# Performance work log

Hardware: AMD Instinct MI355X
Metric: run time of the kernel (lower is better)

The kernel has to match this reference:

```python
import jax, jax.numpy as jnp
import numpy as np

B, T, C = 2, 2048, 1024
NUM_HEADS = 16
HEAD_DIM = C // NUM_HEADS
TEMP = 1.0
LN_EPS = 1e-6


def setup_inputs() -> dict:
    key = jax.random.key(0)
    kx, kqw, kpw = jax.random.split(key, 3)
    x = jax.random.normal(kx, (B, T, C), dtype=jnp.float32)
    # causal mask, broadcastable to [B, H, T, T]
    mask = jnp.tril(jnp.ones((T, T), dtype=bool))[None, None, :, :]
    # LayerNorm params (flax defaults: scale=1, bias=0)
    ln_scale = jnp.ones((C,), dtype=jnp.float32)
    ln_bias = jnp.zeros((C,), dtype=jnp.float32)
    # xavier_uniform init for dense kernels, zero bias (torch_linear)
    lim_qkv = float(np.sqrt(6.0 / (C + 3 * C)))
    qkv_w = jax.random.uniform(kqw, (C, 3 * C), jnp.float32, -lim_qkv, lim_qkv)
    qkv_b = jnp.zeros((3 * C,), dtype=jnp.float32)
    lim_p = float(np.sqrt(6.0 / (C + C)))
    proj_w = jax.random.uniform(kpw, (C, C), jnp.float32, -lim_p, lim_p)
    proj_b = jnp.zeros((C,), dtype=jnp.float32)
    return {"x": x, "mask": mask, "ln_scale": ln_scale, "ln_bias": ln_bias,
            "qkv_w": qkv_w, "qkv_b": qkv_b, "proj_w": proj_w, "proj_b": proj_b}


def reference(x, mask, ln_scale, ln_bias, qkv_w, qkv_b, proj_w, proj_b):
    b, t, c = x.shape
    # LayerNorm (eps=1e-6, flax default)
    mu = jnp.mean(x, axis=-1, keepdims=True)
    var = jnp.mean(jnp.square(x - mu), axis=-1, keepdims=True)
    xn = (x - mu) * jax.lax.rsqrt(var + LN_EPS) * ln_scale + ln_bias
    # fused QKV projection
    qkv = xn @ qkv_w + qkv_b
    q, k, v = jnp.split(qkv, 3, axis=-1)
    q = q.reshape(b, t, NUM_HEADS, HEAD_DIM) / TEMP
    k = k.reshape(b, t, NUM_HEADS, HEAD_DIM)
    v = v.reshape(b, t, NUM_HEADS, HEAD_DIM)
    # scaled dot-product attention with mask (eval path: no dropout)
    q = q / jnp.sqrt(jnp.float32(HEAD_DIM)).astype(x.dtype)
    scores = jnp.einsum('bqhd,bkhd->bhqk', q, k)  # [B,H,T,T]
    big_neg = jnp.finfo(x.dtype).min
    scores = jnp.where(mask, scores, big_neg)
    attn_weights = jax.nn.softmax(scores, axis=-1).astype(x.dtype)
    out = jnp.einsum('bhqk,bkhd->bqhd', attn_weights, v).reshape(b, t, c)
    return out @ proj_w + proj_b
```

## Files before the change

kernel.cpp:

```cpp
#include <hip/hip_runtime.h>
#include <cstdint>

#define DEV __device__ __forceinline__

typedef unsigned int u32;
typedef unsigned short u16;
typedef __attribute__((ext_vector_type(4))) float f32x4;
typedef __attribute__((ext_vector_type(4))) u32 u32x4;
typedef __attribute__((ext_vector_type(2))) u32 u32x2;
typedef __attribute__((ext_vector_type(8))) __bf16 bf16x8;

static_assert(sizeof(bf16x8) == 16, "bf16x8 must be 16B");

static constexpr int Tn = 2048, Cn = 1024;
static constexpr int Mrows = 2 * Tn;

DEV u16 f2bf_rne(float f) {
  u32 u = __builtin_bit_cast(u32, f);
  u32 r = u + 0x7fffu + ((u >> 16) & 1u);
  return (u16)(r >> 16);
}
DEV float bf2f(u16 h) {
  u32 u = ((u32)h) << 16;
  return __builtin_bit_cast(float, u);
}
DEV u32 pack2bf(float a, float b) {
  return (u32)f2bf_rne(a) | ((u32)f2bf_rne(b) << 16);
}

DEV void stage16(const void* g, void* l) {
#if __has_builtin(__builtin_amdgcn_global_load_lds)
  __builtin_amdgcn_global_load_lds(
      (__attribute__((address_space(1))) u32*)(uintptr_t)g,
      (__attribute__((address_space(3))) u32*)l, 16, 0, 0);
#else
  *(u32x4*)l = *(const u32x4*)g;
#endif
}

__global__ __launch_bounds__(256) void ln_kernel(const float* __restrict__ x,
                                                 const float* __restrict__ sc,
                                                 const float* __restrict__ bi,
                                                 u16* __restrict__ xn) {
  int row = blockIdx.x;
  int t = threadIdx.x;
  const float* xr = x + (size_t)row * Cn;
  f32x4 v = *(const f32x4*)(xr + t * 4);
  float s = v.x + v.y + v.z + v.w;
  float s2 = v.x * v.x + v.y * v.y + v.z * v.z + v.w * v.w;
#pragma unroll
  for (int off = 1; off < 64; off <<= 1) {
    s += __shfl_xor(s, off);
    s2 += __shfl_xor(s2, off);
  }
  __shared__ float red[8];
  if ((t & 63) == 0) {
    red[(t >> 6) * 2] = s;
    red[(t >> 6) * 2 + 1] = s2;
  }
  __syncthreads();
  s = red[0] + red[2] + red[4] + red[6];
  s2 = red[1] + red[3] + red[5] + red[7];
  float mean = s * (1.0f / Cn);
  float var = s2 * (1.0f / Cn) - mean * mean;
  float rstd = rsqrtf(var + 1e-6f);
  f32x4 g = *(const f32x4*)(sc + t * 4);
  f32x4 b = *(const f32x4*)(bi + t * 4);
  u32 lo = pack2bf((v.x - mean) * rstd * g.x + b.x, (v.y - mean) * rstd * g.y + b.y);
  u32 hi = pack2bf((v.z - mean) * rstd * g.z + b.z, (v.w - mean) * rstd * g.w + b.w);
  u32x2 pack = {lo, hi};
  *(u32x2*)(xn + (size_t)row * Cn + t * 4) = pack;
}

__global__ __launch_bounds__(256) void transpose_cast(const float* __restrict__ src,
                                                      u16* __restrict__ dst,
                                                      int R, int Cc) {
  __shared__ float tile[32][33];
  int tx = threadIdx.x, ty = threadIdx.y;
  int c0 = blockIdx.x * 32, r0 = blockIdx.y * 32;
#pragma unroll
  for (int k = 0; k < 4; ++k)
    tile[ty + 8 * k][tx] = src[(size_t)(r0 + ty + 8 * k) * Cc + c0 + tx];
  __syncthreads();
#pragma unroll
  for (int k = 0; k < 4; ++k)
    dst[(size_t)(c0 + ty + 8 * k) * R + r0 + tx] = f2bf_rne(tile[tx][ty + 8 * k]);
}

__global__ __launch_bounds__(256) void vt_prep(const u16* __restrict__ qkvm,
                                               u16* __restrict__ vt) {
  __shared__ u16 tile[32][33];
  int bh = blockIdx.z;
  int b = bh >> 4, h = bh & 15;
  int t0 = blockIdx.x * 32, d0 = blockIdx.y * 32;
  int tx = threadIdx.x, ty = threadIdx.y;
#pragma unroll
  for (int k = 0; k < 4; ++k)
    tile[ty + 8 * k][tx] =
        qkvm[(size_t)(b * Tn + t0 + ty + 8 * k) * 3072 + 2 * Cn + h * 64 + d0 + tx];
  __syncthreads();
#pragma unroll
  for (int k = 0; k < 4; ++k)
    vt[((size_t)bh * 64 + d0 + ty + 8 * k) * 2048 + t0 + tx] = tile[tx][ty + 8 * k];
}

template <bool OUT_F32, bool QKV_SCALE>
__global__ __launch_bounds__(256, 2) void gemm_kernel(const u16* __restrict__ A,
                                                      const u16* __restrict__ Bt,
                                                      const float* __restrict__ bias,
                                                      void* __restrict__ Cout,
                                                      int Nsz, int Ksz) {
  __shared__ u16 As[128 * 32];
  __shared__ u16 Bs[128 * 32];
  int t = threadIdx.x;
  int l = t & 63, w = t >> 6;
  int quad = l >> 4, c16 = l & 15;
  int wm = w & 1, wn = w >> 1;
  int m0 = blockIdx.y * 128, n0 = blockIdx.x * 128;

  f32x4 acc[4][4];
#pragma unroll
  for (int mt = 0; mt < 4; ++mt)
#pragma unroll
    for (int nt = 0; nt < 4; ++nt) acc[mt][nt] = (f32x4){0.f, 0.f, 0.f, 0.f};

  for (int kk = 0; kk < Ksz; kk += 32) {
#pragma unroll
    for (int i = 0; i < 2; ++i) {
      int c = t + i * 256;
      int m = c >> 2, k8 = (c & 3) ^ ((m >> 1) & 3);
      stage16(A + (size_t)(m0 + m) * Ksz + kk + k8 * 8, (char*)As + c * 16);
    }
#pragma unroll
    for (int i = 0; i < 2; ++i) {
      int c = t + i * 256;
      int n = c >> 2, k8 = (c & 3) ^ ((n >> 1) & 3);
      stage16(Bt + (size_t)(n0 + n) * Ksz + kk + k8 * 8, (char*)Bs + c * 16);
    }
    __syncthreads();
    bf16x8 af[4], bf[4];
#pragma unroll
    for (int mt = 0; mt < 4; ++mt) {
      int m = wm * 64 + mt * 16 + c16;
      int LC = m * 4 + (quad ^ ((m >> 1) & 3));
      af[mt] = *(const bf16x8*)((const char*)As + LC * 16);
    }
#pragma unroll
    for (int nt = 0; nt < 4; ++nt) {
      int n = wn * 64 + nt * 16 + c16;
      int LC = n * 4 + (quad ^ ((n >> 1) & 3));
      bf[nt] = *(const bf16x8*)((const char*)Bs + LC * 16);
    }
#pragma unroll
    for (int mt = 0; mt < 4; ++mt)
#pragma unroll
      for (int nt = 0; nt < 4; ++nt)
        acc[mt][nt] = __builtin_amdgcn_mfma_f32_16x16x32_bf16(af[mt], bf[nt],
                                                              acc[mt][nt], 0, 0, 0);
    __syncthreads();
  }
#pragma unroll
  for (int mt = 0; mt < 4; ++mt) {
    int row = m0 + wm * 64 + mt * 16 + quad * 4;
#pragma unroll
    for (int nt = 0; nt < 4; ++nt) {
      int col = n0 + wn * 64 + nt * 16 + c16;
      float bv = bias[col];
      float scale = (QKV_SCALE && col < 1024) ? 0.125f : 1.0f;
#pragma unroll
      for (int r = 0; r < 4; ++r) {
        float v = (acc[mt][nt][r] + bv) * scale;
        if (OUT_F32)
          ((float*)Cout)[(size_t)(row + r) * Nsz + col] = v;
        else
          ((u16*)Cout)[(size_t)(row + r) * Nsz + col] = f2bf_rne(v);
      }
    }
  }
}

__constant__ int4 chunk_tab[24] = {
    {15, 0, 8, 0}, {15, 8, 8, 1}, {14, 0, 8, 0}, {7, 0, 8, -1},
    {14, 8, 7, 1}, {13, 0, 7, 0}, {13, 7, 7, 1}, {12, 0, 7, 0}, {6, 0, 7, -1},
    {12, 7, 6, 1}, {11, 0, 6, 0}, {11, 6, 6, 1}, {10, 0, 6, 0}, {5, 0, 6, -1},
    {10, 6, 5, 1}, {9, 0, 5, 0}, {9, 5, 5, 1}, {8, 0, 5, 0}, {4, 0, 5, -1},
    {8, 5, 4, 1}, {3, 0, 4, -1},
    {2, 0, 3, -1},
    {1, 0, 2, -1},
    {0, 0, 1, -1}};

__global__ __launch_bounds__(256, 2) void flash_kernel(const u16* __restrict__ qkv,
                                                       const u16* __restrict__ vt,
                                                       u16* __restrict__ aout,
                                                       u16* __restrict__ Op,
                                                       float* __restrict__ ml) {
  int4 ck = chunk_tab[blockIdx.x >> 5];
  int bh = blockIdx.x & 31;
  int qt = ck.x, k0 = ck.y, kend = ck.y + ck.z, half = ck.w;
  int b = bh >> 4, h = bh & 15;
  int t = threadIdx.x, l = t & 63, w = t >> 6;
  int quad = l >> 4, c16 = l & 15;
  int q0 = qt * 128;

  __shared__ u16 Ks[128 * 64];
  __shared__ u16 Vs[64 * 128];
  __shared__ u16 Ps[128 * 128];

  bf16x8 qf[2][2];
#pragma unroll
  for (int nt = 0; nt < 2; ++nt)
#pragma unroll
    for (int ks = 0; ks < 2; ++ks)
      qf[nt][ks] = *(const bf16x8*)(qkv +
          (size_t)(b * Tn + q0 + w * 32 + nt * 16 + c16) * 3072 +
          h * 64 + ks * 32 + quad * 8);

  float mrow[2] = {-1e30f, -1e30f};
  float lrow[2] = {0.f, 0.f};
  f32x4 o[2][4];
#pragma unroll
  for (int mq = 0; mq < 2; ++mq)
#pragma unroll
    for (int dt = 0; dt < 4; ++dt) o[mq][dt] = (f32x4){0.f, 0.f, 0.f, 0.f};

  for (int kt = k0; kt < kend; ++kt) {
#pragma unroll
    for (int i = 0; i < 4; ++i) {
      int c = t + i * 256;
      int key = c >> 3, d8 = (c & 7) ^ (key & 7);
      stage16(qkv + (size_t)(b * Tn + kt * 128 + key) * 3072 + Cn + h * 64 + d8 * 8,
              (char*)Ks + c * 16);
    }
#pragma unroll
    for (int i = 0; i < 4; ++i) {
      int c = t + i * 256;
      int d = c >> 4, k8 = (c & 15) ^ (d & 15);
      stage16(vt + ((size_t)bh * 64 + d) * 2048 + kt * 128 + k8 * 8,
              (char*)Vs + c * 16);
    }
    __syncthreads();

    f32x4 s[8][2];
#pragma unroll
    for (int mt = 0; mt < 8; ++mt)
#pragma unroll
      for (int nt = 0; nt < 2; ++nt) s[mt][nt] = (f32x4){0.f, 0.f, 0.f, 0.f};
#pragma unroll
    for (int mt = 0; mt < 8; ++mt) {
#pragma unroll
      for (int ks = 0; ks < 2; ++ks) {
        int key = mt * 16 + c16;
        int d8 = ks * 4 + quad;
        int LC = key * 8 + (d8 ^ (key & 7));
        bf16x8 kf = *(const bf16x8*)((const char*)Ks + LC * 16);
#pragma unroll
        for (int nt = 0; nt < 2; ++nt)
          s[mt][nt] = __builtin_amdgcn_mfma_f32_16x16x32_bf16(kf, qf[nt][ks],
                                                              s[mt][nt], 0, 0, 0);
      }
    }
    if (kt == qt) {
#pragma unroll
      for (int mt = 0; mt < 8; ++mt)
#pragma unroll
        for (int nt = 0; nt < 2; ++nt)
#pragma unroll
          for (int r = 0; r < 4; ++r) {
            int key = kt * 128 + mt * 16 + quad * 4 + r;
            int q = q0 + w * 32 + nt * 16 + c16;
            if (key > q) s[mt][nt][r] = -1e30f;
          }
    }
    float alph[2];
#pragma unroll
    for (int nt = 0; nt < 2; ++nt) {
      float rm = -1e30f;
#pragma unroll
      for (int mt = 0; mt < 8; ++mt)
#pragma unroll
        for (int r = 0; r < 4; ++r) rm = fmaxf(rm, s[mt][nt][r]);
      rm = fmaxf(rm, __shfl_xor(rm, 16));
      rm = fmaxf(rm, __shfl_xor(rm, 32));
      float mnew = fmaxf(mrow[nt], rm);
      alph[nt] = __expf(mrow[nt] - mnew);
      mrow[nt] = mnew;
      float rs = 0.f;
#pragma unroll
      for (int mt = 0; mt < 8; ++mt)
#pragma unroll
        for (int r = 0; r < 4; ++r) {
          float e = __expf(s[mt][nt][r] - mnew);
          s[mt][nt][r] = e;
          rs += e;
        }
      rs += __shfl_xor(rs, 16);
      rs += __shfl_xor(rs, 32);
      lrow[nt] = lrow[nt] * alph[nt] + rs;
    }
#pragma unroll
    for (int mq = 0; mq < 2; ++mq)
#pragma unroll
      for (int r = 0; r < 4; ++r) {
        float a = __shfl(alph[mq], quad * 4 + r);
#pragma unroll
        for (int dt = 0; dt < 4; ++dt) o[mq][dt][r] *= a;
      }
#pragma unroll
    for (int mt = 0; mt < 8; ++mt)
#pragma unroll
      for (int nt = 0; nt < 2; ++nt) {
        int q = w * 32 + nt * 16 + c16;
        int kc = mt * 4 + quad;
        int LC = q * 32 + (kc ^ ((q & 15) << 1));
        u32x2 pk = {pack2bf(s[mt][nt][0], s[mt][nt][1]),
                    pack2bf(s[mt][nt][2], s[mt][nt][3])};
        *(u32x2*)((char*)Ps + LC * 8) = pk;
      }
#pragma unroll
    for (int ks = 0; ks < 4; ++ks) {
      bf16x8 pa[2];
#pragma unroll
      for (int mq = 0; mq < 2; ++mq) {
        int q = w * 32 + mq * 16 + c16;
        int kc = ks * 8 + quad * 2;
        int LC = q * 32 + (kc ^ ((q & 15) << 1));
        pa[mq] = *(const bf16x8*)((const char*)Ps + LC * 8);
      }
#pragma unroll
      for (int dt = 0; dt < 4; ++dt) {
        int d = dt * 16 + c16;
        int vc = d * 16 + ((ks * 4 + quad) ^ (d & 15));
        bf16x8 vf = *(const bf16x8*)((const char*)Vs + vc * 16);
#pragma unroll
        for (int mq = 0; mq < 2; ++mq)
          o[mq][dt] = __builtin_amdgcn_mfma_f32_16x16x32_bf16(pa[mq], vf, o[mq][dt],
                                                              0, 0, 0);
      }
    }
    __syncthreads();
  }

  float linv[2] = {1.0f / lrow[0], 1.0f / lrow[1]};
  if (half < 0) {
#pragma unroll
    for (int mq = 0; mq < 2; ++mq)
#pragma unroll
      for (int r = 0; r < 4; ++r) {
        float li = __shfl(linv[mq], quad * 4 + r);
        int q = q0 + w * 32 + mq * 16 + quad * 4 + r;
#pragma unroll
        for (int dt = 0; dt < 4; ++dt)
          aout[(size_t)(b * Tn + q) * 1024 + h * 64 + dt * 16 + c16] =
              f2bf_rne(o[mq][dt][r] * li);
      }
  } else {
    int ps = ((qt - 8) * 32 + bh) * 2 + half;
#pragma unroll
    for (int mq = 0; mq < 2; ++mq)
#pragma unroll
      for (int r = 0; r < 4; ++r) {
        float li = __shfl(linv[mq], quad * 4 + r);
        int qr = w * 32 + mq * 16 + quad * 4 + r;
#pragma unroll
        for (int dt = 0; dt < 4; ++dt)
          Op[((size_t)ps * 128 + qr) * 64 + dt * 16 + c16] =
              f2bf_rne(o[mq][dt][r] * li);
      }
    if (quad == 0) {
#pragma unroll
      for (int nt = 0; nt < 2; ++nt) {
        int qr = w * 32 + nt * 16 + c16;
        ml[((size_t)ps * 128 + qr) * 2] = mrow[nt];
        ml[((size_t)ps * 128 + qr) * 2 + 1] = lrow[nt];
      }
    }
  }
}

__global__ __launch_bounds__(256) void combine_kernel(const u16* __restrict__ Op,
                                                      const float* __restrict__ ml,
                                                      u16* __restrict__ aout) {
  int qt = 8 + (blockIdx.x >> 5);
  int bh = blockIdx.x & 31;
  int b = bh >> 4, h = bh & 15;
  int ps0 = ((qt - 8) * 32 + bh) * 2;
  int d = threadIdx.x & 63, rq = threadIdx.x >> 6;
  for (int r = 0; r < 32; ++r) {
    int row = rq * 32 + r;
    float m0 = ml[((size_t)ps0 * 128 + row) * 2];
    float l0 = ml[((size_t)ps0 * 128 + row) * 2 + 1];
    float m1 = ml[((size_t)(ps0 + 1) * 128 + row) * 2];
    float l1 = ml[((size_t)(ps0 + 1) * 128 + row) * 2 + 1];
    float M = fmaxf(m0, m1);
    float w0 = __expf(m0 - M) * l0, w1 = __expf(m1 - M) * l1;
    float inv = 1.0f / (w0 + w1);
    float o0 = bf2f(Op[((size_t)ps0 * 128 + row) * 64 + d]);
    float o1 = bf2f(Op[((size_t)(ps0 + 1) * 128 + row) * 64 + d]);
    aout[(size_t)(b * Tn + qt * 128 + row) * 1024 + h * 64 + d] =
        f2bf_rne((w0 * o0 + w1 * o1) * inv);
  }
}

extern "C" void kernel_launch(void* const* d_in, const int* in_sizes, int n_in,
                              void* d_out, int out_size, void* d_ws, size_t ws_size,
                              hipStream_t stream) {
  const float* x = (const float*)d_in[0];
  const float* ln_s = (const float*)d_in[2];
  const float* ln_b = (const float*)d_in[3];
  const float* qkv_w = (const float*)d_in[4];
  const float* qkv_b = (const float*)d_in[5];
  const float* proj_w = (const float*)d_in[6];
  const float* proj_b = (const float*)d_in[7];
  float* out = (float*)d_out;
  char* ws = (char*)d_ws;

  u16* xn = (u16*)ws;
  u16* wqkv = (u16*)(ws + (8ull << 20));
  u16* wproj = (u16*)(ws + (14ull << 20));
  u16* qkvm = (u16*)(ws + (16ull << 20));
  u16* attn = (u16*)(ws + (40ull << 20));
  u16* vt = (u16*)(ws + (48ull << 20));
  u16* Op = (u16*)ws;
  float* ml = (float*)(ws + (8ull << 20));

  ln_kernel<<<Mrows, 256, 0, stream>>>(x, ln_s, ln_b, xn);
  transpose_cast<<<dim3(96, 32), dim3(32, 8), 0, stream>>>(qkv_w, wqkv, 1024, 3072);
  transpose_cast<<<dim3(32, 32), dim3(32, 8), 0, stream>>>(proj_w, wproj, 1024, 1024);
  gemm_kernel<false, true><<<dim3(24, 32), 256, 0, stream>>>(xn, wqkv, qkv_b, qkvm,
                                                             3072, 1024);
  vt_prep<<<dim3(64, 2, 32), dim3(32, 8), 0, stream>>>(qkvm, vt);
  flash_kernel<<<768, 256, 0, stream>>>(qkvm, vt, attn, Op, ml);
  combine_kernel<<<256, 256, 0, stream>>>(Op, ml, attn);
  gemm_kernel<true, false><<<dim3(8, 32), 256, 0, stream>>>(attn, wproj, proj_b, out,
                                                            1024, 1024);
}
```

Before: 224.1 us.

## Halve P buffer, use exp2 softmax, merge weight transposes, raise occupancy

The softmax P tile in shared memory is halved by writing and consuming it in two half-key chunks, cutting LDS use so the launch bounds can ask for 3 blocks per CU in both the flash and GEMM kernels. The log2(e) factor is folded into the Q scale so softmax can use the hardware exp2. The two weight transpose launches are merged into one. Asking for higher occupancy tightens the register budget and may cause spills, and the chunked P path adds LDS round trips and barriers per tile.

Result: slower. 239.8 us (+7.0%).

```diff
diff --git a/kernel.cpp b/kernel.cpp
--- a/kernel.cpp
+++ b/kernel.cpp
@@ -1,5 +1,6 @@
 #include <hip/hip_runtime.h>
 #include <cstdint>
+#include <math.h>
 
 #define DEV __device__ __forceinline__
 
@@ -14,6 +15,7 @@
 
 static constexpr int Tn = 2048, Cn = 1024;
 static constexpr int Mrows = 2 * Tn;
+static constexpr float QSCALE2 = 0.125f * 1.44269504088896f;
 
 DEV u16 f2bf_rne(float f) {
   u32 u = __builtin_bit_cast(u32, f);
@@ -26,6 +28,13 @@
 }
 DEV u32 pack2bf(float a, float b) {
   return (u32)f2bf_rne(a) | ((u32)f2bf_rne(b) << 16);
+}
+DEV float fexp2(float x) {
+#if __has_builtin(__builtin_amdgcn_exp2f)
+  return __builtin_amdgcn_exp2f(x);
+#else
+  return exp2f(x);
+#endif
 }
 
 DEV void stage16(const void* g, void* l) {
@@ -72,19 +81,29 @@
   *(u32x2*)(xn + (size_t)row * Cn + t * 4) = pack;
 }
 
-__global__ __launch_bounds__(256) void transpose_cast(const float* __restrict__ src,
-                                                      u16* __restrict__ dst,
-                                                      int R, int Cc) {
+__global__ __launch_bounds__(256) void transpose_cast2(const float* __restrict__ qkv_w,
+                                                       u16* __restrict__ wqkv,
+                                                       const float* __restrict__ proj_w,
+                                                       u16* __restrict__ wproj) {
   __shared__ float tile[32][33];
+  int bx = blockIdx.x;
+  const float* src;
+  u16* dst;
+  int Cc;
+  if (bx < 96) {
+    src = qkv_w; dst = wqkv; Cc = 3072;
+  } else {
+    src = proj_w; dst = wproj; Cc = 1024; bx -= 96;
+  }
   int tx = threadIdx.x, ty = threadIdx.y;
-  int c0 = blockIdx.x * 32, r0 = blockIdx.y * 32;
+  int c0 = bx * 32, r0 = blockIdx.y * 32;
 #pragma unroll
   for (int k = 0; k < 4; ++k)
     tile[ty + 8 * k][tx] = src[(size_t)(r0 + ty + 8 * k) * Cc + c0 + tx];
   __syncthreads();
 #pragma unroll
   for (int k = 0; k < 4; ++k)
-    dst[(size_t)(c0 + ty + 8 * k) * R + r0 + tx] = f2bf_rne(tile[tx][ty + 8 * k]);
+    dst[(size_t)(c0 + ty + 8 * k) * 1024 + r0 + tx] = f2bf_rne(tile[tx][ty + 8 * k]);
 }
 
 __global__ __launch_bounds__(256) void vt_prep(const u16* __restrict__ qkvm,
@@ -105,7 +124,7 @@
 }
 
 template <bool OUT_F32, bool QKV_SCALE>
-__global__ __launch_bounds__(256, 2) void gemm_kernel(const u16* __restrict__ A,
+__global__ __launch_bounds__(256, 3) void gemm_kernel(const u16* __restrict__ A,
                                                       const u16* __restrict__ Bt,
                                                       const float* __restrict__ bias,
                                                       void* __restrict__ Cout,
@@ -166,7 +185,7 @@
     for (int nt = 0; nt < 4; ++nt) {
       int col = n0 + wn * 64 + nt * 16 + c16;
       float bv = bias[col];
-      float scale = (QKV_SCALE && col < 1024) ? 0.125f : 1.0f;
+      float scale = (QKV_SCALE && col < 1024) ? QSCALE2 : 1.0f;
 #pragma unroll
       for (int r = 0; r < 4; ++r) {
         float v = (acc[mt][nt][r] + bv) * scale;
@@ -189,7 +208,7 @@
     {1, 0, 2, -1},
     {0, 0, 1, -1}};
 
-__global__ __launch_bounds__(256, 2) void flash_kernel(const u16* __restrict__ qkv,
+__global__ __launch_bounds__(256, 3) void flash_kernel(const u16* __restrict__ qkv,
                                                        const u16* __restrict__ vt,
                                                        u16* __restrict__ aout,
                                                        u16* __restrict__ Op,
@@ -204,7 +223,7 @@
 
   __shared__ u16 Ks[128 * 64];
   __shared__ u16 Vs[64 * 128];
-  __shared__ u16 Ps[128 * 128];
+  __shared__ u16 Ps[128 * 64];
 
   bf16x8 qf[2][2];
 #pragma unroll
@@ -282,14 +301,14 @@
       rm = fmaxf(rm, __shfl_xor(rm, 16));
       rm = fmaxf(rm, __shfl_xor(rm, 32));
       float mnew = fmaxf(mrow[nt], rm);
-      alph[nt] = __expf(mrow[nt] - mnew);
+      alph[nt] = fexp2(mrow[nt] - mnew);
       mrow[nt] = mnew;
       float rs = 0.f;
 #pragma unroll
       for (int mt = 0; mt < 8; ++mt)
 #pragma unroll
         for (int r = 0; r < 4; ++r) {
-          float e = __expf(s[mt][nt][r] - mnew);
+          float e = fexp2(s[mt][nt][r] - mnew);
           s[mt][nt][r] = e;
           rs += e;
         }
@@ -306,35 +325,41 @@
         for (int dt = 0; dt < 4; ++dt) o[mq][dt][r] *= a;
       }
 #pragma unroll
-    for (int mt = 0; mt < 8; ++mt)
-#pragma unroll
-      for (int nt = 0; nt < 2; ++nt) {
-        int q = w * 32 + nt * 16 + c16;
-        int kc = mt * 4 + quad;
-        int LC = q * 32 + (kc ^ ((q & 15) << 1));
-        u32x2 pk = {pack2bf(s[mt][nt][0], s[mt][nt][1]),
-                    pack2bf(s[mt][nt][2], s[mt][nt][3])};
-        *(u32x2*)((char*)Ps + LC * 8) = pk;
-      }
-#pragma unroll
-    for (int ks = 0; ks < 4; ++ks) {
-      bf16x8 pa[2];
-#pragma unroll
-      for (int mq = 0; mq < 2; ++mq) {
-        int q = w * 32 + mq * 16 + c16;
-        int kc = ks * 8 + quad * 2;
-        int LC = q * 32 + (kc ^ ((q & 15) << 1));
-        pa[mq] = *(const bf16x8*)((const char*)Ps + LC * 8);
-      }
-#pragma unroll
-      for (int dt = 0; dt < 4; ++dt) {
-        int d = dt * 16 + c16;
-        int vc = d * 16 + ((ks * 4 + quad) ^ (d & 15));
-        bf16x8 vf = *(const bf16x8*)((const char*)Vs + vc * 16);
-#pragma unroll
-        for (int mq = 0; mq < 2; ++mq)
-          o[mq][dt] = __builtin_amdgcn_mfma_f32_16x16x32_bf16(pa[mq], vf, o[mq][dt],
-                                                              0, 0, 0);
+    for (int ksh = 0; ksh < 2; ++ksh) {
+#pragma unroll
+      for (int mtl = 0; mtl < 4; ++mtl) {
+        int mt = ksh * 4 + mtl;
+#pragma unroll
+        for (int nt = 0; nt < 2; ++nt) {
+          int q = w * 32 + nt * 16 + c16;
+          int c8 = mtl * 2 + (quad >> 1);
+          u32x2 pk = {pack2bf(s[mt][nt][0], s[mt][nt][1]),
+                      pack2bf(s[mt][nt][2], s[mt][nt][3])};
+          *(u32x2*)((char*)Ps + q * 128 + ((c8 ^ (c16 & 7)) * 16) + (quad & 1) * 8) =
+              pk;
+        }
+      }
+#pragma unroll
+      for (int ksl = 0; ksl < 2; ++ksl) {
+        int ks = ksh * 2 + ksl;
+        bf16x8 pa[2];
+#pragma unroll
+        for (int mq = 0; mq < 2; ++mq) {
+          int q = w * 32 + mq * 16 + c16;
+          int c8 = ksl * 4 + quad;
+          pa[mq] = *(const bf16x8*)((const char*)Ps + q * 128 +
+                                    ((c8 ^ (c16 & 7)) * 16));
+        }
+#pragma unroll
+        for (int dt = 0; dt < 4; ++dt) {
+          int d = dt * 16 + c16;
+          int vc = d * 16 + ((ks * 4 + quad) ^ (d & 15));
+          bf16x8 vf = *(const bf16x8*)((const char*)Vs + vc * 16);
+#pragma unroll
+          for (int mq = 0; mq < 2; ++mq)
+            o[mq][dt] = __builtin_amdgcn_mfma_f32_16x16x32_bf16(pa[mq], vf,
+                                                                o[mq][dt], 0, 0, 0);
+        }
       }
     }
     __syncthreads();
@@ -392,7 +417,7 @@
     float m1 = ml[((size_t)(ps0 + 1) * 128 + row) * 2];
     float l1 = ml[((size_t)(ps0 + 1) * 128 + row) * 2 + 1];
     float M = fmaxf(m0, m1);
-    float w0 = __expf(m0 - M) * l0, w1 = __expf(m1 - M) * l1;
+    float w0 = fexp2(m0 - M) * l0, w1 = fexp2(m1 - M) * l1;
     float inv = 1.0f / (w0 + w1);
     float o0 = bf2f(Op[((size_t)ps0 * 128 + row) * 64 + d]);
     float o1 = bf2f(Op[((size_t)(ps0 + 1) * 128 + row) * 64 + d]);
@@ -424,8 +449,8 @@
   float* ml = (float*)(ws + (8ull << 20));
 
   ln_kernel<<<Mrows, 256, 0, stream>>>(x, ln_s, ln_b, xn);
-  transpose_cast<<<dim3(96, 32), dim3(32, 8), 0, stream>>>(qkv_w, wqkv, 1024, 3072);
-  transpose_cast<<<dim3(32, 32), dim3(32, 8), 0, stream>>>(proj_w, wproj, 1024, 1024);
+  transpose_cast2<<<dim3(128, 32), dim3(32, 8), 0, stream>>>(qkv_w, wqkv, proj_w,
+                                                             wproj);
   gemm_kernel<false, true><<<dim3(24, 32), 256, 0, stream>>>(xn, wqkv, qkv_b, qkvm,
                                                              3072, 1024);
   vt_prep<<<dim3(64, 2, 32), dim3(32, 8), 0, stream>>>(qkvm, vt);
```
